# Performance work log

Measured on AMD Instinct MI355X. Metric: run time of the kernel, lower is better.

Reference implementation:

```python
import jax, jax.numpy as jnp
import numpy as np

N, E, D, L = 50000, 800000, 96, 4
IN_H, IN_E, HID, OUT = 26, 4, 128, 8
BN_EPS, AGG_EPS = 1e-5, 1e-6


def setup_inputs() -> dict:
    key = jax.random.key(0)
    ks = jax.random.split(key, 24)
    f32 = jnp.float32
    nrm = lambda k, sh, s=0.05: jax.random.normal(k, sh, f32) * s
    inp = {
        "h1": nrm(ks[0], (N, 6), 1.0),
        "h2": nrm(ks[1], (N, 4), 1.0),
        "z": nrm(ks[2], (N, 16), 1.0),
        "efeat": nrm(ks[3], (E, IN_E), 1.0),
        "max_action": jnp.ones((N, 1), f32),
        "Wh_emb": nrm(ks[4], (IN_H, D)), "bh_emb": jnp.zeros((D,), f32),
        "We_emb": nrm(ks[5], (IN_E, D)), "be_emb": jnp.zeros((D,), f32),
        "WA": nrm(ks[6], (L, D, D)), "bA": jnp.zeros((L, D), f32),
        "WB": nrm(ks[7], (L, D, D)), "bB": jnp.zeros((L, D), f32),
        "WC": nrm(ks[8], (L, D, D)), "bC": jnp.zeros((L, D), f32),
        "WD": nrm(ks[9], (L, D, D)), "bD": jnp.zeros((L, D), f32),
        "WE": nrm(ks[10], (L, D, D)), "bE": jnp.zeros((L, D), f32),
        "bn_h_g": jnp.ones((L, D), f32), "bn_h_b": jnp.zeros((L, D), f32),
        "bn_e_g": jnp.ones((L, D), f32), "bn_e_b": jnp.zeros((L, D), f32),
        "W1": nrm(ks[11], (D, HID)), "b1": jnp.zeros((HID,), f32),
        "W2": nrm(ks[12], (HID, OUT)), "b2": jnp.zeros((OUT,), f32),
        "src": jax.random.randint(ks[13], (E,), 0, N),
        "dst": jax.random.randint(ks[14], (E,), 0, N),
    }
    return inp


def _bn(x, g, b):
    # BatchNorm1d in train mode: batch stats over node/edge axis, biased var
    mu = x.mean(axis=0)
    var = x.var(axis=0)
    return g * (x - mu) * jax.lax.rsqrt(var + BN_EPS) + b


def reference(h1, h2, z, efeat, max_action, Wh_emb, bh_emb, We_emb, be_emb,
              WA, bA, WB, bB, WC, bC, WD, bD, WE, bE,
              bn_h_g, bn_h_b, bn_e_g, bn_e_b, W1, b1, W2, b2, src, dst):
    # input embedding  (Actor concat: states then z)
    h = jnp.concatenate([h1, h2, z], axis=-1) @ Wh_emb + bh_emb   # [N, D]
    e = efeat @ We_emb + be_emb                                    # [E, D]
    n = h.shape[0]
    for l in range(L):  # GatedGCN layers (residual + BN + ReLU)
        Ah = h @ WA[l] + bA[l]
        Bh = h @ WB[l] + bB[l]
        Dh = h @ WD[l] + bD[l]
        Eh = h @ WE[l] + bE[l]
        Ce = e @ WC[l] + bC[l]
        e_new = Dh[src] + Eh[dst] + Ce                             # [E, D]
        sig = jax.nn.sigmoid(e_new)
        num = jax.ops.segment_sum(sig * Bh[src], dst, num_segments=n)
        den = jax.ops.segment_sum(sig, dst, num_segments=n)
        h_new = Ah + num / (den + AGG_EPS)
        h = h + jax.nn.relu(_bn(h_new, bn_h_g[l], bn_h_b[l]))
        e = e + jax.nn.relu(_bn(e_new, bn_e_g[l], bn_e_b[l]))
    # MLP head + tanh scale
    out = jax.nn.relu(h @ W1 + b1) @ W2 + b2                        # [N, OUT]
    return max_action * jnp.tanh(out)
```

## Files before the change

kernel.cpp:

```cpp
#include <hip/hip_runtime.h>
#include <math.h>

#define NN 50000
#define EE 800000
#define DD 96
#define NHID 128
#define NOUT 8
#define LDA 104

typedef unsigned int uint32;
typedef float floatx2 __attribute__((ext_vector_type(2)));
typedef float f32x4 __attribute__((ext_vector_type(4)));
typedef short bf16x8 __attribute__((ext_vector_type(8)));

__device__ __forceinline__ float bfu2f(ushort u) {
  union { uint32 u; float f; } v; v.u = ((uint32)u) << 16; return v.f;
}
__device__ __forceinline__ ushort f2bf(float x) {
  union { float f; uint32 u; } v; v.f = x;
  uint32 r = (v.u + 0x7fffu + ((v.u >> 16) & 1u)) >> 16;
  return (ushort)r;
}

template <int ESZ> struct EST;
template <> struct EST<2> {
  static __device__ __forceinline__ float4 ld(const void* e, size_t grp) {
    const ushort4 a = ((const ushort4*)e)[grp];
    return make_float4(bfu2f(a.x), bfu2f(a.y), bfu2f(a.z), bfu2f(a.w));
  }
  static __device__ __forceinline__ void st(void* e, size_t grp, float4 v) {
    ushort4 o; o.x = f2bf(v.x); o.y = f2bf(v.y); o.z = f2bf(v.z); o.w = f2bf(v.w);
    ((ushort4*)e)[grp] = o;
  }
  static __device__ __forceinline__ float ld1c(const void* e, size_t pos, int c) {
    return bfu2f(((const ushort*)e)[pos * DD + c]);
  }
};
template <> struct EST<1> {
  static __device__ __forceinline__ float4 ld(const void* e, size_t grp) {
    const int u = ((const int*)e)[grp];
    floatx2 lo = __builtin_amdgcn_cvt_pk_f32_fp8(u, false);
    floatx2 hi = __builtin_amdgcn_cvt_pk_f32_fp8(u, true);
    return make_float4(lo[0], lo[1], hi[0], hi[1]);
  }
  static __device__ __forceinline__ void st(void* e, size_t grp, float4 v) {
    int u = 0;
    u = __builtin_amdgcn_cvt_pk_fp8_f32(v.x, v.y, u, false);
    u = __builtin_amdgcn_cvt_pk_fp8_f32(v.z, v.w, u, true);
    ((int*)e)[grp] = u;
  }
  static __device__ __forceinline__ float ld1c(const void* e, size_t pos, int c) {
    const int dw = ((const int*)e)[pos * (DD / 4) + (c >> 2)];
    floatx2 lo = __builtin_amdgcn_cvt_pk_f32_fp8(dw, false);
    floatx2 hi = __builtin_amdgcn_cvt_pk_f32_fp8(dw, true);
    return (c & 2) ? ((c & 1) ? hi[1] : hi[0]) : ((c & 1) ? lo[1] : lo[0]);
  }
};

__global__ __launch_bounds__(256) void k_zero_init(int* __restrict__ cnt,
    float* __restrict__ stats) {
  int i = blockIdx.x * 256 + threadIdx.x;
  const int str = gridDim.x * 256;
  for (; i < NN; i += str) cnt[i] = 0;
  if (blockIdx.x == 0)
    for (int j = threadIdx.x; j < 768; j += 256) stats[j] = 0.f;
}

__global__ __launch_bounds__(256) void k_hist(const int* __restrict__ dst,
    int* __restrict__ cnt) {
  const int i = blockIdx.x * 256 + threadIdx.x;
  if (i < EE) atomicAdd(&cnt[dst[i]], 1);
}

__global__ __launch_bounds__(256) void k_scan(const int* __restrict__ cnt,
    int* __restrict__ rowptr, int* __restrict__ cursor) {
  __shared__ int part[256];
  const int t = threadIdx.x;
  const int CH = (NN + 255) / 256;
  const int lo = t * CH, hi = min((t + 1) * CH, NN);
  int s = 0;
  for (int i = lo; i < hi; i++) s += cnt[i];
  part[t] = s;
  __syncthreads();
  for (int off = 1; off < 256; off <<= 1) {
    int v = (t >= off) ? part[t - off] : 0;
    __syncthreads();
    part[t] += v;
    __syncthreads();
  }
  int base = (t == 0) ? 0 : part[t - 1];
  for (int i = lo; i < hi; i++) {
    rowptr[i] = base; cursor[i] = base; base += cnt[i];
  }
  if (t == 255) rowptr[NN] = base;
}

__global__ __launch_bounds__(256) void k_scatter(const int* __restrict__ src,
    const int* __restrict__ dst, int* __restrict__ cursor,
    int* __restrict__ perm, int* __restrict__ srcC, int* __restrict__ dstC) {
  const int i = blockIdx.x * 256 + threadIdx.x;
  if (i < EE) {
    const int d = dst[i];
    const int pos = atomicAdd(&cursor[d], 1);
    perm[pos] = i; srcC[pos] = src[i]; dstC[pos] = d;
  }
}

__global__ __launch_bounds__(256) void k_embed_h(const float* __restrict__ h1,
    const float* __restrict__ h2, const float* __restrict__ z,
    const float* __restrict__ W, const float* __restrict__ b,
    ushort* __restrict__ h) {
  int idx = blockIdx.x * 256 + threadIdx.x;
  const int total = NN * DD;
  const int stride = gridDim.x * 256;
  for (; idx < total; idx += stride) {
    int n = idx / DD, c = idx - n * DD;
    float acc = b[c];
#pragma unroll
    for (int k = 0; k < 6; k++)  acc = fmaf(h1[n * 6 + k], W[k * DD + c], acc);
#pragma unroll
    for (int k = 0; k < 4; k++)  acc = fmaf(h2[n * 4 + k], W[(6 + k) * DD + c], acc);
#pragma unroll
    for (int k = 0; k < 16; k++) acc = fmaf(z[n * 16 + k], W[(10 + k) * DD + c], acc);
    h[idx] = f2bf(acc);
  }
}

template <int EZ>
__global__ __launch_bounds__(256) void k_embed_e(const float* __restrict__ ef,
    const float* __restrict__ W, const float* __restrict__ b,
    const int* __restrict__ perm, void* __restrict__ e) {
  int g = blockIdx.x * 256 + threadIdx.x;
  const int totalg = EE * (DD / 4);
  const int stride = gridDim.x * 256;
  for (; g < totalg; g += stride) {
    const int pos = g / 24, cg = (g - pos * 24) * 4;
    const int orig = perm[pos];
    const float f0 = ef[orig * 4], f1 = ef[orig * 4 + 1];
    const float f2 = ef[orig * 4 + 2], f3 = ef[orig * 4 + 3];
    float4 acc;
    acc.x = b[cg+0] + f0*W[cg+0] + f1*W[DD+cg+0] + f2*W[2*DD+cg+0] + f3*W[3*DD+cg+0];
    acc.y = b[cg+1] + f0*W[cg+1] + f1*W[DD+cg+1] + f2*W[2*DD+cg+1] + f3*W[3*DD+cg+1];
    acc.z = b[cg+2] + f0*W[cg+2] + f1*W[DD+cg+2] + f2*W[2*DD+cg+2] + f3*W[3*DD+cg+2];
    acc.w = b[cg+3] + f0*W[cg+3] + f1*W[DD+cg+3] + f2*W[2*DD+cg+3] + f3*W[3*DD+cg+3];
    EST<EZ>::st(e, g, acc);
  }
}

__global__ __launch_bounds__(256) void k_ngemm(const ushort* __restrict__ h,
    const float* __restrict__ WAp, const float* __restrict__ WBp,
    const float* __restrict__ WDp, const float* __restrict__ WEp,
    const float* __restrict__ bAp, const float* __restrict__ bBp,
    const float* __restrict__ bDp, const float* __restrict__ bEp,
    ushort* __restrict__ oA, ushort* __restrict__ oB,
    ushort* __restrict__ oD, ushort* __restrict__ oE) {
  const float* W; const float* bias; ushort* out;
  const int m = blockIdx.y;
  if (m == 0)      { W = WAp; bias = bAp; out = oA; }
  else if (m == 1) { W = WBp; bias = bBp; out = oB; }
  else if (m == 2) { W = WDp; bias = bDp; out = oD; }
  else             { W = WEp; bias = bEp; out = oE; }
  __shared__ __align__(16) ushort Wt[DD * LDA];
  __shared__ __align__(16) ushort At[64 * LDA];
  const int tid = threadIdx.x;
  for (int i = tid; i < DD * DD; i += 256) {
    const int k = i / DD, n = i - (i / DD) * DD;
    Wt[n * LDA + k] = f2bf(W[i]);
  }
  const int base = blockIdx.x * 64;
  for (int i = tid; i < 64 * 24; i += 256) {
    const int r = i / 24, q = i - (i / 24) * 24;
    const int row = base + r;
    ushort4 a;
    if (row < NN) a = ((const ushort4*)h)[(size_t)row * 24 + q];
    else { a.x = 0; a.y = 0; a.z = 0; a.w = 0; }
    *(ushort4*)&At[r * LDA + q * 4] = a;
  }
  __syncthreads();
  const int w = tid >> 6, lane = tid & 63;
  const int lrow = lane & 15, lgrp = lane >> 4;
  f32x4 acc[6];
#pragma unroll
  for (int nt = 0; nt < 6; nt++) { acc[nt][0]=0.f; acc[nt][1]=0.f; acc[nt][2]=0.f; acc[nt][3]=0.f; }
#pragma unroll
  for (int kk = 0; kk < 3; kk++) {
    const bf16x8 af = *(const bf16x8*)&At[(w * 16 + lrow) * LDA + kk * 32 + lgrp * 8];
#pragma unroll
    for (int nt = 0; nt < 6; nt++) {
      const bf16x8 bfr = *(const bf16x8*)&Wt[(nt * 16 + lrow) * LDA + kk * 32 + lgrp * 8];
      acc[nt] = __builtin_amdgcn_mfma_f32_16x16x32_bf16(af, bfr, acc[nt], 0, 0, 0);
    }
  }
#pragma unroll
  for (int j = 0; j < 4; j++) {
    const int row = base + w * 16 + lgrp * 4 + j;
    if (row < NN) {
#pragma unroll
      for (int nt = 0; nt < 6; nt++) {
        const int ch = nt * 16 + lrow;
        out[(size_t)row * DD + ch] = f2bf(acc[nt][j] + bias[ch]);
      }
    }
  }
}

template <int MODE, int EZE, int EZN>
__global__ __launch_bounds__(256) void k_edge(void* __restrict__ e,
    void* __restrict__ e_new,
    const float* __restrict__ WC, const float* __restrict__ bC,
    const ushort* __restrict__ Dh, const ushort* __restrict__ Eh,
    const int* __restrict__ srcC, const int* __restrict__ dstC,
    float* __restrict__ stats) {
  __shared__ __align__(16) ushort Wt[DD * LDA];
  __shared__ __align__(16) ushort At[64 * LDA];
  __shared__ float sred[2 * DD];
  __shared__ float escl[DD], eshl[DD];
  __shared__ int sidx_s[64], sidx_d[64];
  const int tid = threadIdx.x;
  for (int i = tid; i < DD * DD; i += 256) {
    const int k = i / DD, n = i - (i / DD) * DD;
    Wt[n * LDA + k] = f2bf(WC[i]);
  }
  if (tid < 2 * DD) sred[tid] = 0.f;
  if (MODE >= 1 && tid < DD) { escl[tid] = stats[576 + tid]; eshl[tid] = stats[672 + tid]; }
  __syncthreads();
  const int w = tid >> 6, lane = tid & 63;
  const int lrow = lane & 15, lgrp = lane >> 4;
  const int qq0 = lane % 24;
  const int qq1 = (lane + 16) % 24;
  const int qq2 = (lane + 8) % 24;
  const float4 bc0 = *(const float4*)&bC[qq0 * 4];
  const float4 bc1 = *(const float4*)&bC[qq1 * 4];
  const float4 bc2 = *(const float4*)&bC[qq2 * 4];
  float sacc0[4] = {0,0,0,0}, sacc1[4] = {0,0,0,0}, sacc2[4] = {0,0,0,0};
  float qacc0[4] = {0,0,0,0}, qacc1[4] = {0,0,0,0}, qacc2[4] = {0,0,0,0};

  const int NT = EE / 64;
  for (int t = blockIdx.x; t < NT; t += gridDim.x) {
    const size_t base = (size_t)t * 64;
#pragma unroll
    for (int ii = 0; ii < 6; ii++) {
      const int i = ii * 256 + tid;
      const int r = i / 24, gq = i - (i / 24) * 24;
      const size_t gi = (base + r) * 24 + gq;
      float4 a = EST<EZE>::ld(e, gi);
      if (MODE >= 1) {
        const float4 d = EST<EZN>::ld(e_new, gi);
        const int c = gq * 4;
        a.x += fmaxf(fmaf(d.x, escl[c],     eshl[c]),     0.f);
        a.y += fmaxf(fmaf(d.y, escl[c + 1], eshl[c + 1]), 0.f);
        a.z += fmaxf(fmaf(d.z, escl[c + 2], eshl[c + 2]), 0.f);
        a.w += fmaxf(fmaf(d.w, escl[c + 3], eshl[c + 3]), 0.f);
        if (MODE == 1) EST<EZE>::st(e, gi, a);
      }
      ushort4 o; o.x = f2bf(a.x); o.y = f2bf(a.y); o.z = f2bf(a.z); o.w = f2bf(a.w);
      *(ushort4*)&At[r * LDA + gq * 4] = o;
    }
    if (tid < 64) { sidx_s[tid] = srcC[base + tid]; sidx_d[tid] = dstC[base + tid]; }
    __syncthreads();
    f32x4 acc[6];
#pragma unroll
    for (int nt = 0; nt < 6; nt++) { acc[nt][0]=0.f; acc[nt][1]=0.f; acc[nt][2]=0.f; acc[nt][3]=0.f; }
#pragma unroll
    for (int kk = 0; kk < 3; kk++) {
      const bf16x8 af = *(const bf16x8*)&At[(w * 16 + lrow) * LDA + kk * 32 + lgrp * 8];
#pragma unroll
      for (int nt = 0; nt < 6; nt++) {
        const bf16x8 bfr = *(const bf16x8*)&Wt[(nt * 16 + lrow) * LDA + kk * 32 + lgrp * 8];
        acc[nt] = __builtin_amdgcn_mfma_f32_16x16x32_bf16(af, bfr, acc[nt], 0, 0, 0);
      }
    }
#pragma unroll
    for (int j = 0; j < 4; j++) {
#pragma unroll
      for (int nt = 0; nt < 6; nt++) {
        At[(w * 16 + lgrp * 4 + j) * LDA + nt * 16 + lrow] = f2bf(acc[nt][j]);
      }
    }
#pragma unroll
    for (int it = 0; it < 6; it++) {
      const int idx = it * 64 + lane;
      const int r16 = idx / 24, gq = idx - r16 * 24;
      const int row = w * 16 + r16;
      const size_t pos = base + row;
      const int s = sidx_s[row], d2 = sidx_d[row];
      const ushort4 av = *(const ushort4*)&At[row * LDA + gq * 4];
      const ushort4 dv = *(const ushort4*)&Dh[(size_t)s * DD + gq * 4];
      const ushort4 ev = *(const ushort4*)&Eh[(size_t)d2 * DD + gq * 4];
      const float4 bc = (it % 3 == 0) ? bc0 : (it % 3 == 1) ? bc1 : bc2;
      float4 v;
      v.x = bfu2f(av.x) + bc.x + bfu2f(dv.x) + bfu2f(ev.x);
      v.y = bfu2f(av.y) + bc.y + bfu2f(dv.y) + bfu2f(ev.y);
      v.z = bfu2f(av.z) + bc.z + bfu2f(dv.z) + bfu2f(ev.z);
      v.w = bfu2f(av.w) + bc.w + bfu2f(dv.w) + bfu2f(ev.w);
      if (it % 3 == 0) {
        sacc0[0]+=v.x; sacc0[1]+=v.y; sacc0[2]+=v.z; sacc0[3]+=v.w;
        qacc0[0]+=v.x*v.x; qacc0[1]+=v.y*v.y; qacc0[2]+=v.z*v.z; qacc0[3]+=v.w*v.w;
      } else if (it % 3 == 1) {
        sacc1[0]+=v.x; sacc1[1]+=v.y; sacc1[2]+=v.z; sacc1[3]+=v.w;
        qacc1[0]+=v.x*v.x; qacc1[1]+=v.y*v.y; qacc1[2]+=v.z*v.z; qacc1[3]+=v.w*v.w;
      } else {
        sacc2[0]+=v.x; sacc2[1]+=v.y; sacc2[2]+=v.z; sacc2[3]+=v.w;
        qacc2[0]+=v.x*v.x; qacc2[1]+=v.y*v.y; qacc2[2]+=v.z*v.z; qacc2[3]+=v.w*v.w;
      }
      EST<EZN>::st(e_new, pos * 24 + gq, v);
    }
    __syncthreads();
  }
#pragma unroll
  for (int c = 0; c < 4; c++) {
    atomicAdd(&sred[qq0 * 4 + c], sacc0[c]);
    atomicAdd(&sred[DD + qq0 * 4 + c], qacc0[c]);
    atomicAdd(&sred[qq1 * 4 + c], sacc1[c]);
    atomicAdd(&sred[DD + qq1 * 4 + c], qacc1[c]);
    atomicAdd(&sred[qq2 * 4 + c], sacc2[c]);
    atomicAdd(&sred[DD + qq2 * 4 + c], qacc2[c]);
  }
  __syncthreads();
  if (tid < 2 * DD) atomicAdd(&stats[tid], sred[tid]);
}

template <int EZN>
__global__ __launch_bounds__(256) void k_agg(const void* __restrict__ e_new,
    const int* __restrict__ srcC, const int* __restrict__ rowptr,
    const ushort* __restrict__ Bh, ushort* __restrict__ hn,
    float* __restrict__ stats) {
  __shared__ float sred[2 * DD];
  if (threadIdx.x < 2 * DD) sred[threadIdx.x] = 0.f;
  __syncthreads();
  const int hw = threadIdx.x >> 5, lane = threadIdx.x & 31;
  const int c0 = lane, c1 = lane + 32, c2 = lane + 64;
  float sa0 = 0, sa1 = 0, sa2 = 0, qa0 = 0, qa1 = 0, qa2 = 0;
  for (int n = blockIdx.x * 8 + hw; n < NN; n += gridDim.x * 8) {
    const int rs = rowptr[n], re = rowptr[n + 1];
    float n0 = 0, n1 = 0, n2 = 0, d0 = 0, d1 = 0, d2 = 0;
    for (int p = rs; p < re; p++) {
      const int s = srcC[p];
      const float v0 = EST<EZN>::ld1c(e_new, (size_t)p, c0);
      const float v1 = EST<EZN>::ld1c(e_new, (size_t)p, c1);
      const float v2 = EST<EZN>::ld1c(e_new, (size_t)p, c2);
      const float g0 = 1.f / (1.f + __expf(-v0));
      const float g1 = 1.f / (1.f + __expf(-v1));
      const float g2 = 1.f / (1.f + __expf(-v2));
      const size_t sb = (size_t)s * DD;
      n0 += g0 * bfu2f(Bh[sb + c0]); d0 += g0;
      n1 += g1 * bfu2f(Bh[sb + c1]); d1 += g1;
      n2 += g2 * bfu2f(Bh[sb + c2]); d2 += g2;
    }
    const size_t hb = (size_t)n * DD;
    const float v0 = bfu2f(hn[hb + c0]) + n0 / (d0 + 1e-6f);
    const float v1 = bfu2f(hn[hb + c1]) + n1 / (d1 + 1e-6f);
    const float v2 = bfu2f(hn[hb + c2]) + n2 / (d2 + 1e-6f);
    hn[hb + c0] = f2bf(v0); hn[hb + c1] = f2bf(v1); hn[hb + c2] = f2bf(v2);
    sa0 += v0; qa0 += v0 * v0;
    sa1 += v1; qa1 += v1 * v1;
    sa2 += v2; qa2 += v2 * v2;
  }
  atomicAdd(&sred[c0], sa0); atomicAdd(&sred[c1], sa1); atomicAdd(&sred[c2], sa2);
  atomicAdd(&sred[DD + c0], qa0); atomicAdd(&sred[DD + c1], qa1); atomicAdd(&sred[DD + c2], qa2);
  __syncthreads();
  if (threadIdx.x < 2 * DD) atomicAdd(&stats[192 + threadIdx.x], sred[threadIdx.x]);
}

__global__ void k_finalize(float* __restrict__ stats,
    const float* __restrict__ g_h, const float* __restrict__ b_h,
    const float* __restrict__ g_e, const float* __restrict__ b_e) {
  const int c = threadIdx.x;
  if (c < DD) {
    const float mu_h = stats[192 + c] / (float)NN;
    const float var_h = stats[288 + c] / (float)NN - mu_h * mu_h;
    const float sc_h = g_h[c] * rsqrtf(var_h + 1e-5f);
    const float mu_e = stats[c] / (float)EE;
    const float var_e = stats[96 + c] / (float)EE - mu_e * mu_e;
    const float sc_e = g_e[c] * rsqrtf(var_e + 1e-5f);
    stats[384 + c] = sc_h;
    stats[480 + c] = b_h[c] - mu_h * sc_h;
    stats[576 + c] = sc_e;
    stats[672 + c] = b_e[c] - mu_e * sc_e;
    stats[c] = 0.f; stats[96 + c] = 0.f; stats[192 + c] = 0.f; stats[288 + c] = 0.f;
  }
}

__global__ __launch_bounds__(256) void k_update_h(ushort* __restrict__ h,
    const ushort* __restrict__ hn, const float* __restrict__ stats) {
  int idx = blockIdx.x * 256 + threadIdx.x;
  const int stride = gridDim.x * 256;
  for (; idx < NN * DD; idx += stride) {
    const int c = idx % DD;
    const float v = fmaf(bfu2f(hn[idx]), stats[384 + c], stats[480 + c]);
    h[idx] = f2bf(bfu2f(h[idx]) + fmaxf(v, 0.f));
  }
}

__global__ __launch_bounds__(256) void k_head(const ushort* __restrict__ h,
    const float* __restrict__ W1, const float* __restrict__ b1,
    const float* __restrict__ W2, const float* __restrict__ b2,
    const float* __restrict__ ma, float* __restrict__ out) {
  __shared__ float W1l[DD * NHID];
  __shared__ float W2l[NHID * NOUT];
  __shared__ float hid[4][NHID];
  __shared__ float hrow[4][DD];
  for (int i = threadIdx.x; i < DD * NHID; i += 256) W1l[i] = W1[i];
  for (int i = threadIdx.x; i < NHID * NOUT; i += 256) W2l[i] = W2[i];
  __syncthreads();
  const int w = threadIdx.x >> 6, lane = threadIdx.x & 63;
  for (int n = blockIdx.x * 4 + w; n < NN; n += gridDim.x * 4) {
    const ushort* hp = h + (size_t)n * DD;
    if (lane < DD - 64) hrow[w][64 + lane] = bfu2f(hp[64 + lane]);
    hrow[w][lane] = bfu2f(hp[lane]);
    float a0 = b1[lane], a1 = b1[64 + lane];
    for (int k = 0; k < DD; k++) {
      const float x = hrow[w][k];
      a0 = fmaf(x, W1l[k * NHID + lane], a0);
      a1 = fmaf(x, W1l[k * NHID + 64 + lane], a1);
    }
    hid[w][lane] = fmaxf(a0, 0.f);
    hid[w][64 + lane] = fmaxf(a1, 0.f);
    if (lane < NOUT) {
      float o = b2[lane];
      for (int k = 0; k < NHID; k++) o = fmaf(hid[w][k], W2l[k * NOUT + lane], o);
      out[(size_t)n * NOUT + lane] = ma[n] * tanhf(o);
    }
  }
}

extern "C" void kernel_launch(void* const* d_in, const int* in_sizes, int n_in,
                              void* d_out, int out_size, void* d_ws, size_t ws_size,
                              hipStream_t stream) {
  const float* h1  = (const float*)d_in[0];
  const float* h2  = (const float*)d_in[1];
  const float* z   = (const float*)d_in[2];
  const float* ef  = (const float*)d_in[3];
  const float* ma  = (const float*)d_in[4];
  const float* Wh  = (const float*)d_in[5];
  const float* bh  = (const float*)d_in[6];
  const float* We  = (const float*)d_in[7];
  const float* be  = (const float*)d_in[8];
  const float* WA  = (const float*)d_in[9];
  const float* bA  = (const float*)d_in[10];
  const float* WB  = (const float*)d_in[11];
  const float* bB  = (const float*)d_in[12];
  const float* WC  = (const float*)d_in[13];
  const float* bC  = (const float*)d_in[14];
  const float* WD  = (const float*)d_in[15];
  const float* bD  = (const float*)d_in[16];
  const float* WE  = (const float*)d_in[17];
  const float* bE  = (const float*)d_in[18];
  const float* bn_h_g = (const float*)d_in[19];
  const float* bn_h_b = (const float*)d_in[20];
  const float* bn_e_g = (const float*)d_in[21];
  const float* bn_e_b = (const float*)d_in[22];
  const float* W1  = (const float*)d_in[23];
  const float* b1  = (const float*)d_in[24];
  const float* W2  = (const float*)d_in[25];
  const float* b2  = (const float*)d_in[26];
  const int*   src = (const int*)d_in[27];
  const int*   dst = (const int*)d_in[28];

  const size_t E_ELEMS = (size_t)EE * DD;
  const size_t N_ELEMS = (size_t)NN * DD;
  int tier;
  if (ws_size >= 455000000UL)      tier = 0;
  else if (ws_size >= 297000000UL) tier = 1;
  else                             tier = 2;
  const size_t esze = (tier == 0) ? 2 : 1;
  const size_t eszn = (tier <= 1) ? 2 : 1;

  char* p = (char*)d_ws;
  void* e     = (void*)p; p += E_ELEMS * esze;
  void* e_new = (void*)p; p += E_ELEMS * eszn;
  ushort* h   = (ushort*)p; p += N_ELEMS * 2;
  ushort* hn  = (ushort*)p; p += N_ELEMS * 2;
  ushort* Bhb = (ushort*)p; p += N_ELEMS * 2;
  ushort* Dhb = (ushort*)p; p += N_ELEMS * 2;
  ushort* Ehb = (ushort*)p; p += N_ELEMS * 2;
  int* cnt    = (int*)p; p += (size_t)NN * 4;
  int* rowptr = (int*)p; p += (size_t)(NN + 1) * 4;
  int* cursor = (int*)p; p += (size_t)NN * 4;
  int* perm   = (int*)p; p += (size_t)EE * 4;
  int* srcC   = (int*)p; p += (size_t)EE * 4;
  int* dstC   = (int*)p; p += (size_t)EE * 4;
  float* stats = (float*)p;

  k_zero_init<<<64, 256, 0, stream>>>(cnt, stats);
  k_hist<<<3125, 256, 0, stream>>>(dst, cnt);
  k_scan<<<1, 256, 0, stream>>>(cnt, rowptr, cursor);
  k_scatter<<<3125, 256, 0, stream>>>(src, dst, cursor, perm, srcC, dstC);
  k_embed_h<<<1024, 256, 0, stream>>>(h1, h2, z, Wh, bh, h);
  if (esze == 2) k_embed_e<2><<<2048, 256, 0, stream>>>(ef, We, be, perm, e);
  else           k_embed_e<1><<<2048, 256, 0, stream>>>(ef, We, be, perm, e);

  for (int l = 0; l < 4; l++) {
    dim3 gn(782, 4);
    k_ngemm<<<gn, 256, 0, stream>>>(h,
        WA + l * DD * DD, WB + l * DD * DD, WD + l * DD * DD, WE + l * DD * DD,
        bA + l * DD, bB + l * DD, bD + l * DD, bE + l * DD,
        hn, Bhb, Dhb, Ehb);
    const float* WCl = WC + l * DD * DD;
    const float* bCl = bC + l * DD;
#define EDGE_ARGS e, e_new, WCl, bCl, Dhb, Ehb, srcC, dstC, stats
    if (tier == 0) {
      if (l == 0)      k_edge<0,2,2><<<1250, 256, 0, stream>>>(EDGE_ARGS);
      else if (l < 3)  k_edge<1,2,2><<<1250, 256, 0, stream>>>(EDGE_ARGS);
      else             k_edge<2,2,2><<<1250, 256, 0, stream>>>(EDGE_ARGS);
    } else if (tier == 1) {
      if (l == 0)      k_edge<0,1,2><<<1250, 256, 0, stream>>>(EDGE_ARGS);
      else if (l < 3)  k_edge<1,1,2><<<1250, 256, 0, stream>>>(EDGE_ARGS);
      else             k_edge<2,1,2><<<1250, 256, 0, stream>>>(EDGE_ARGS);
    } else {
      if (l == 0)      k_edge<0,1,1><<<1250, 256, 0, stream>>>(EDGE_ARGS);
      else if (l < 3)  k_edge<1,1,1><<<1250, 256, 0, stream>>>(EDGE_ARGS);
      else             k_edge<2,1,1><<<1250, 256, 0, stream>>>(EDGE_ARGS);
    }
#undef EDGE_ARGS
    if (eszn == 2) k_agg<2><<<1024, 256, 0, stream>>>(e_new, srcC, rowptr, Bhb, hn, stats);
    else           k_agg<1><<<1024, 256, 0, stream>>>(e_new, srcC, rowptr, Bhb, hn, stats);
    k_finalize<<<1, 128, 0, stream>>>(stats,
        bn_h_g + l * DD, bn_h_b + l * DD, bn_e_g + l * DD, bn_e_b + l * DD);
    k_update_h<<<1024, 256, 0, stream>>>(h, hn, stats);
  }

  k_head<<<1024, 256, 0, stream>>>(h, W1, b1, W2, b2, ma, (float*)d_out);
}
```

Baseline: 2.057 ms.

## Make edge kernel wave-independent, widen edge loads, unroll aggregation loop by two

```diff
diff --git a/kernel.cpp b/kernel.cpp
--- a/kernel.cpp
+++ b/kernel.cpp
@@ -12,6 +12,7 @@
 typedef float floatx2 __attribute__((ext_vector_type(2)));
 typedef float f32x4 __attribute__((ext_vector_type(4)));
 typedef short bf16x8 __attribute__((ext_vector_type(8)));
+typedef ushort ushort8_t __attribute__((ext_vector_type(8)));
 
 __device__ __forceinline__ float bfu2f(ushort u) {
   union { uint32 u; float f; } v; v.u = ((uint32)u) << 16; return v.f;
@@ -31,6 +32,17 @@
   static __device__ __forceinline__ void st(void* e, size_t grp, float4 v) {
     ushort4 o; o.x = f2bf(v.x); o.y = f2bf(v.y); o.z = f2bf(v.z); o.w = f2bf(v.w);
     ((ushort4*)e)[grp] = o;
+  }
+  static __device__ __forceinline__ void ld8(const void* e, size_t i8, float* a) {
+    const ushort8_t u = ((const ushort8_t*)e)[i8];
+#pragma unroll
+    for (int j = 0; j < 8; j++) a[j] = bfu2f(u[j]);
+  }
+  static __device__ __forceinline__ void st8(void* e, size_t i8, const float* a) {
+    ushort8_t u;
+#pragma unroll
+    for (int j = 0; j < 8; j++) u[j] = f2bf(a[j]);
+    ((ushort8_t*)e)[i8] = u;
   }
   static __device__ __forceinline__ float ld1c(const void* e, size_t pos, int c) {
     return bfu2f(((const ushort*)e)[pos * DD + c]);
@@ -48,6 +60,26 @@
     u = __builtin_amdgcn_cvt_pk_fp8_f32(v.x, v.y, u, false);
     u = __builtin_amdgcn_cvt_pk_fp8_f32(v.z, v.w, u, true);
     ((int*)e)[grp] = u;
+  }
+  static __device__ __forceinline__ void ld8(const void* e, size_t i8, float* a) {
+    const int2 u = ((const int2*)e)[i8];
+    floatx2 l0 = __builtin_amdgcn_cvt_pk_f32_fp8(u.x, false);
+    floatx2 h0 = __builtin_amdgcn_cvt_pk_f32_fp8(u.x, true);
+    floatx2 l1 = __builtin_amdgcn_cvt_pk_f32_fp8(u.y, false);
+    floatx2 h1 = __builtin_amdgcn_cvt_pk_f32_fp8(u.y, true);
+    a[0]=l0[0]; a[1]=l0[1]; a[2]=h0[0]; a[3]=h0[1];
+    a[4]=l1[0]; a[5]=l1[1]; a[6]=h1[0]; a[7]=h1[1];
+  }
+  static __device__ __forceinline__ void st8(void* e, size_t i8, const float* a) {
+    int2 u;
+    int w0 = 0;
+    w0 = __builtin_amdgcn_cvt_pk_fp8_f32(a[0], a[1], w0, false);
+    w0 = __builtin_amdgcn_cvt_pk_fp8_f32(a[2], a[3], w0, true);
+    int w1 = 0;
+    w1 = __builtin_amdgcn_cvt_pk_fp8_f32(a[4], a[5], w1, false);
+    w1 = __builtin_amdgcn_cvt_pk_fp8_f32(a[6], a[7], w1, true);
+    u.x = w0; u.y = w1;
+    ((int2*)e)[i8] = u;
   }
   static __device__ __forceinline__ float ld1c(const void* e, size_t pos, int c) {
     const int dw = ((const int*)e)[pos * (DD / 4) + (c >> 2)];
@@ -212,10 +244,9 @@
     const int* __restrict__ srcC, const int* __restrict__ dstC,
     float* __restrict__ stats) {
   __shared__ __align__(16) ushort Wt[DD * LDA];
-  __shared__ __align__(16) ushort At[64 * LDA];
+  __shared__ __align__(16) ushort At[4][16 * LDA];
   __shared__ float sred[2 * DD];
   __shared__ float escl[DD], eshl[DD];
-  __shared__ int sidx_s[64], sidx_d[64];
   const int tid = threadIdx.x;
   for (int i = tid; i < DD * DD; i += 256) {
     const int k = i / DD, n = i - (i / DD) * DD;
@@ -235,35 +266,38 @@
   float sacc0[4] = {0,0,0,0}, sacc1[4] = {0,0,0,0}, sacc2[4] = {0,0,0,0};
   float qacc0[4] = {0,0,0,0}, qacc1[4] = {0,0,0,0}, qacc2[4] = {0,0,0,0};
 
-  const int NT = EE / 64;
-  for (int t = blockIdx.x; t < NT; t += gridDim.x) {
-    const size_t base = (size_t)t * 64;
-#pragma unroll
-    for (int ii = 0; ii < 6; ii++) {
-      const int i = ii * 256 + tid;
-      const int r = i / 24, gq = i - (i / 24) * 24;
-      const size_t gi = (base + r) * 24 + gq;
-      float4 a = EST<EZE>::ld(e, gi);
+  const int NTW = EE / 16;
+  const int gwave = blockIdx.x * 4 + w;
+  const int nwave = gridDim.x * 4;
+  for (int t = gwave; t < NTW; t += nwave) {
+    const size_t base = (size_t)t * 16;
+#pragma unroll
+    for (int it = 0; it < 3; it++) {
+      const int idx = it * 64 + lane;
+      const int r = idx / 12, g8 = idx - (idx / 12) * 12;
+      const size_t gi8 = (base + r) * 12 + g8;
+      float a[8];
+      EST<EZE>::ld8(e, gi8, a);
       if (MODE >= 1) {
-        const float4 d = EST<EZN>::ld(e_new, gi);
-        const int c = gq * 4;
-        a.x += fmaxf(fmaf(d.x, escl[c],     eshl[c]),     0.f);
-        a.y += fmaxf(fmaf(d.y, escl[c + 1], eshl[c + 1]), 0.f);
-        a.z += fmaxf(fmaf(d.z, escl[c + 2], eshl[c + 2]), 0.f);
-        a.w += fmaxf(fmaf(d.w, escl[c + 3], eshl[c + 3]), 0.f);
-        if (MODE == 1) EST<EZE>::st(e, gi, a);
+        float d[8];
+        EST<EZN>::ld8(e_new, gi8, d);
+        const int c = g8 * 8;
+#pragma unroll
+        for (int j = 0; j < 8; j++)
+          a[j] += fmaxf(fmaf(d[j], escl[c + j], eshl[c + j]), 0.f);
+        if (MODE == 1) EST<EZE>::st8(e, gi8, a);
       }
-      ushort4 o; o.x = f2bf(a.x); o.y = f2bf(a.y); o.z = f2bf(a.z); o.w = f2bf(a.w);
-      *(ushort4*)&At[r * LDA + gq * 4] = o;
-    }
-    if (tid < 64) { sidx_s[tid] = srcC[base + tid]; sidx_d[tid] = dstC[base + tid]; }
-    __syncthreads();
+      ushort8_t o;
+#pragma unroll
+      for (int j = 0; j < 8; j++) o[j] = f2bf(a[j]);
+      *(ushort8_t*)&At[w][r * LDA + g8 * 8] = o;
+    }
     f32x4 acc[6];
 #pragma unroll
     for (int nt = 0; nt < 6; nt++) { acc[nt][0]=0.f; acc[nt][1]=0.f; acc[nt][2]=0.f; acc[nt][3]=0.f; }
 #pragma unroll
     for (int kk = 0; kk < 3; kk++) {
-      const bf16x8 af = *(const bf16x8*)&At[(w * 16 + lrow) * LDA + kk * 32 + lgrp * 8];
+      const bf16x8 af = *(const bf16x8*)&At[w][lrow * LDA + kk * 32 + lgrp * 8];
 #pragma unroll
       for (int nt = 0; nt < 6; nt++) {
         const bf16x8 bfr = *(const bf16x8*)&Wt[(nt * 16 + lrow) * LDA + kk * 32 + lgrp * 8];
@@ -274,17 +308,16 @@
     for (int j = 0; j < 4; j++) {
 #pragma unroll
       for (int nt = 0; nt < 6; nt++) {
-        At[(w * 16 + lgrp * 4 + j) * LDA + nt * 16 + lrow] = f2bf(acc[nt][j]);
+        At[w][(lgrp * 4 + j) * LDA + nt * 16 + lrow] = f2bf(acc[nt][j]);
       }
     }
 #pragma unroll
     for (int it = 0; it < 6; it++) {
       const int idx = it * 64 + lane;
-      const int r16 = idx / 24, gq = idx - r16 * 24;
-      const int row = w * 16 + r16;
-      const size_t pos = base + row;
-      const int s = sidx_s[row], d2 = sidx_d[row];
-      const ushort4 av = *(const ushort4*)&At[row * LDA + gq * 4];
+      const int r16 = idx / 24, gq = idx - (idx / 24) * 24;
+      const size_t pos = base + r16;
+      const int s = srcC[pos], d2 = dstC[pos];
+      const ushort4 av = *(const ushort4*)&At[w][r16 * LDA + gq * 4];
       const ushort4 dv = *(const ushort4*)&Dh[(size_t)s * DD + gq * 4];
       const ushort4 ev = *(const ushort4*)&Eh[(size_t)d2 * DD + gq * 4];
       const float4 bc = (it % 3 == 0) ? bc0 : (it % 3 == 1) ? bc1 : bc2;
@@ -305,7 +338,6 @@
       }
       EST<EZN>::st(e_new, pos * 24 + gq, v);
     }
-    __syncthreads();
   }
 #pragma unroll
   for (int c = 0; c < 4; c++) {
@@ -334,7 +366,29 @@
   for (int n = blockIdx.x * 8 + hw; n < NN; n += gridDim.x * 8) {
     const int rs = rowptr[n], re = rowptr[n + 1];
     float n0 = 0, n1 = 0, n2 = 0, d0 = 0, d1 = 0, d2 = 0;
-    for (int p = rs; p < re; p++) {
+    int p = rs;
+    for (; p + 2 <= re; p += 2) {
+      const int sA = srcC[p], sB = srcC[p + 1];
+      const float vA0 = EST<EZN>::ld1c(e_new, (size_t)p, c0);
+      const float vA1 = EST<EZN>::ld1c(e_new, (size_t)p, c1);
+      const float vA2 = EST<EZN>::ld1c(e_new, (size_t)p, c2);
+      const float vB0 = EST<EZN>::ld1c(e_new, (size_t)(p + 1), c0);
+      const float vB1 = EST<EZN>::ld1c(e_new, (size_t)(p + 1), c1);
+      const float vB2 = EST<EZN>::ld1c(e_new, (size_t)(p + 1), c2);
+      const size_t sbA = (size_t)sA * DD, sbB = (size_t)sB * DD;
+      const float bA0 = bfu2f(Bh[sbA + c0]), bA1 = bfu2f(Bh[sbA + c1]), bA2 = bfu2f(Bh[sbA + c2]);
+      const float bB0 = bfu2f(Bh[sbB + c0]), bB1 = bfu2f(Bh[sbB + c1]), bB2 = bfu2f(Bh[sbB + c2]);
+      const float gA0 = 1.f / (1.f + __expf(-vA0));
+      const float gA1 = 1.f / (1.f + __expf(-vA1));
+      const float gA2 = 1.f / (1.f + __expf(-vA2));
+      const float gB0 = 1.f / (1.f + __expf(-vB0));
+      const float gB1 = 1.f / (1.f + __expf(-vB1));
+      const float gB2 = 1.f / (1.f + __expf(-vB2));
+      n0 += gA0 * bA0 + gB0 * bB0; d0 += gA0 + gB0;
+      n1 += gA1 * bA1 + gB1 * bB1; d1 += gA1 + gB1;
+      n2 += gA2 * bA2 + gB2 * bB2; d2 += gA2 + gB2;
+    }
+    if (p < re) {
       const int s = srcC[p];
       const float v0 = EST<EZN>::ld1c(e_new, (size_t)p, c0);
       const float v1 = EST<EZN>::ld1c(e_new, (size_t)p, c1);
@@ -500,17 +554,17 @@
     const float* bCl = bC + l * DD;
 #define EDGE_ARGS e, e_new, WCl, bCl, Dhb, Ehb, srcC, dstC, stats
     if (tier == 0) {
-      if (l == 0)      k_edge<0,2,2><<<1250, 256, 0, stream>>>(EDGE_ARGS);
-      else if (l < 3)  k_edge<1,2,2><<<1250, 256, 0, stream>>>(EDGE_ARGS);
-      else             k_edge<2,2,2><<<1250, 256, 0, stream>>>(EDGE_ARGS);
+      if (l == 0)      k_edge<0,2,2><<<2500, 256, 0, stream>>>(EDGE_ARGS);
+      else if (l < 3)  k_edge<1,2,2><<<2500, 256, 0, stream>>>(EDGE_ARGS);
+      else             k_edge<2,2,2><<<2500, 256, 0, stream>>>(EDGE_ARGS);
     } else if (tier == 1) {
-      if (l == 0)      k_edge<0,1,2><<<1250, 256, 0, stream>>>(EDGE_ARGS);
-      else if (l < 3)  k_edge<1,1,2><<<1250, 256, 0, stream>>>(EDGE_ARGS);
-      else             k_edge<2,1,2><<<1250, 256, 0, stream>>>(EDGE_ARGS);
+      if (l == 0)      k_edge<0,1,2><<<2500, 256, 0, stream>>>(EDGE_ARGS);
+      else if (l < 3)  k_edge<1,1,2><<<2500, 256, 0, stream>>>(EDGE_ARGS);
+      else             k_edge<2,1,2><<<2500, 256, 0, stream>>>(EDGE_ARGS);
     } else {
-      if (l == 0)      k_edge<0,1,1><<<1250, 256, 0, stream>>>(EDGE_ARGS);
-      else if (l < 3)  k_edge<1,1,1><<<1250, 256, 0, stream>>>(EDGE_ARGS);
-      else             k_edge<2,1,1><<<1250, 256, 0, stream>>>(EDGE_ARGS);
+      if (l == 0)      k_edge<0,1,1><<<2500, 256, 0, stream>>>(EDGE_ARGS);
+      else if (l < 3)  k_edge<1,1,1><<<2500, 256, 0, stream>>>(EDGE_ARGS);
+      else             k_edge<2,1,1><<<2500, 256, 0, stream>>>(EDGE_ARGS);
     }
 #undef EDGE_ARGS
     if (eszn == 2) k_agg<2><<<1024, 256, 0, stream>>>(e_new, srcC, rowptr, Bhb, hn, stats);
```

Result: slower. 2.949 ms (+43.4%).

## Fuse BN residual update into node GEMM and head, merge four GEMMs per block

Applied to the files above, without the earlier changes.

```diff
diff --git a/kernel.cpp b/kernel.cpp
--- a/kernel.cpp
+++ b/kernel.cpp
@@ -147,60 +147,97 @@
   }
 }
 
-__global__ __launch_bounds__(256) void k_ngemm(const ushort* __restrict__ h,
+template <int LAZY>
+__global__ __launch_bounds__(256) void k_ngemm(ushort* __restrict__ h,
     const float* __restrict__ WAp, const float* __restrict__ WBp,
     const float* __restrict__ WDp, const float* __restrict__ WEp,
     const float* __restrict__ bAp, const float* __restrict__ bBp,
     const float* __restrict__ bDp, const float* __restrict__ bEp,
     ushort* __restrict__ oA, ushort* __restrict__ oB,
-    ushort* __restrict__ oD, ushort* __restrict__ oE) {
-  const float* W; const float* bias; ushort* out;
-  const int m = blockIdx.y;
-  if (m == 0)      { W = WAp; bias = bAp; out = oA; }
-  else if (m == 1) { W = WBp; bias = bBp; out = oB; }
-  else if (m == 2) { W = WDp; bias = bDp; out = oD; }
-  else             { W = WEp; bias = bEp; out = oE; }
+    ushort* __restrict__ oD, ushort* __restrict__ oE,
+    const float* __restrict__ stats) {
   __shared__ __align__(16) ushort Wt[DD * LDA];
-  __shared__ __align__(16) ushort At[64 * LDA];
+  __shared__ __align__(16) ushort At[128 * LDA];
+  __shared__ float uscl[DD], ushf[DD];
   const int tid = threadIdx.x;
-  for (int i = tid; i < DD * DD; i += 256) {
-    const int k = i / DD, n = i - (i / DD) * DD;
-    Wt[n * LDA + k] = f2bf(W[i]);
-  }
-  const int base = blockIdx.x * 64;
-  for (int i = tid; i < 64 * 24; i += 256) {
+  if (LAZY && tid < DD) { uscl[tid] = stats[384 + tid]; ushf[tid] = stats[480 + tid]; }
+  if (LAZY) __syncthreads();
+  const int base = blockIdx.x * 128;
+#pragma unroll
+  for (int ii = 0; ii < 12; ii++) {
+    const int i = ii * 256 + tid;
     const int r = i / 24, q = i - (i / 24) * 24;
     const int row = base + r;
-    ushort4 a;
-    if (row < NN) a = ((const ushort4*)h)[(size_t)row * 24 + q];
-    else { a.x = 0; a.y = 0; a.z = 0; a.w = 0; }
+    ushort4 a; a.x = 0; a.y = 0; a.z = 0; a.w = 0;
+    if (row < NN) {
+      a = ((const ushort4*)h)[(size_t)row * 24 + q];
+      if (LAZY) {
+        const ushort4 u = ((const ushort4*)0)[0], *dummy = &u; (void)dummy;
+      }
+    }
+    if (LAZY && row < NN) {
+      const ushort4 u = ((const ushort4*)oA)[(size_t)row * 24 + q];
+      const int c = q * 4;
+      float f0 = bfu2f(a.x) + fmaxf(fmaf(bfu2f(u.x), uscl[c],     ushf[c]),     0.f);
+      float f1 = bfu2f(a.y) + fmaxf(fmaf(bfu2f(u.y), uscl[c + 1], ushf[c + 1]), 0.f);
+      float f2 = bfu2f(a.z) + fmaxf(fmaf(bfu2f(u.z), uscl[c + 2], ushf[c + 2]), 0.f);
+      float f3 = bfu2f(a.w) + fmaxf(fmaf(bfu2f(u.w), uscl[c + 3], ushf[c + 3]), 0.f);
+      a.x = f2bf(f0); a.y = f2bf(f1); a.z = f2bf(f2); a.w = f2bf(f3);
+      ((ushort4*)h)[(size_t)row * 24 + q] = a;
+    }
     *(ushort4*)&At[r * LDA + q * 4] = a;
   }
-  __syncthreads();
   const int w = tid >> 6, lane = tid & 63;
   const int lrow = lane & 15, lgrp = lane >> 4;
-  f32x4 acc[6];
-#pragma unroll
-  for (int nt = 0; nt < 6; nt++) { acc[nt][0]=0.f; acc[nt][1]=0.f; acc[nt][2]=0.f; acc[nt][3]=0.f; }
-#pragma unroll
-  for (int kk = 0; kk < 3; kk++) {
-    const bf16x8 af = *(const bf16x8*)&At[(w * 16 + lrow) * LDA + kk * 32 + lgrp * 8];
-#pragma unroll
-    for (int nt = 0; nt < 6; nt++) {
-      const bf16x8 bfr = *(const bf16x8*)&Wt[(nt * 16 + lrow) * LDA + kk * 32 + lgrp * 8];
-      acc[nt] = __builtin_amdgcn_mfma_f32_16x16x32_bf16(af, bfr, acc[nt], 0, 0, 0);
-    }
-  }
-#pragma unroll
-  for (int j = 0; j < 4; j++) {
-    const int row = base + w * 16 + lgrp * 4 + j;
-    if (row < NN) {
+#pragma unroll
+  for (int m = 0; m < 4; m++) {
+    const float* W  = (m == 0) ? WAp : (m == 1) ? WBp : (m == 2) ? WDp : WEp;
+    const float* bi = (m == 0) ? bAp : (m == 1) ? bBp : (m == 2) ? bDp : bEp;
+    ushort* out     = (m == 0) ? oA  : (m == 1) ? oB  : (m == 2) ? oD  : oE;
+#pragma unroll
+    for (int ii = 0; ii < 36; ii++) {
+      const int i = ii * 256 + tid;
+      const int k = i / DD, n = i - (i / DD) * DD;
+      Wt[n * LDA + k] = f2bf(W[i]);
+    }
+    __syncthreads();
+    f32x4 acc[2][6];
+#pragma unroll
+    for (int rt2 = 0; rt2 < 2; rt2++)
 #pragma unroll
       for (int nt = 0; nt < 6; nt++) {
-        const int ch = nt * 16 + lrow;
-        out[(size_t)row * DD + ch] = f2bf(acc[nt][j] + bias[ch]);
-      }
-    }
+        acc[rt2][nt][0] = 0.f; acc[rt2][nt][1] = 0.f;
+        acc[rt2][nt][2] = 0.f; acc[rt2][nt][3] = 0.f;
+      }
+#pragma unroll
+    for (int rt2 = 0; rt2 < 2; rt2++) {
+      const int rt = w * 2 + rt2;
+#pragma unroll
+      for (int kk = 0; kk < 3; kk++) {
+        const bf16x8 af = *(const bf16x8*)&At[(rt * 16 + lrow) * LDA + kk * 32 + lgrp * 8];
+#pragma unroll
+        for (int nt = 0; nt < 6; nt++) {
+          const bf16x8 bfr = *(const bf16x8*)&Wt[(nt * 16 + lrow) * LDA + kk * 32 + lgrp * 8];
+          acc[rt2][nt] = __builtin_amdgcn_mfma_f32_16x16x32_bf16(af, bfr, acc[rt2][nt], 0, 0, 0);
+        }
+      }
+    }
+#pragma unroll
+    for (int rt2 = 0; rt2 < 2; rt2++) {
+      const int rt = w * 2 + rt2;
+#pragma unroll
+      for (int j = 0; j < 4; j++) {
+        const int row = base + rt * 16 + lgrp * 4 + j;
+        if (row < NN) {
+#pragma unroll
+          for (int nt = 0; nt < 6; nt++) {
+            const int ch = nt * 16 + lrow;
+            out[(size_t)row * DD + ch] = f2bf(acc[rt2][nt][j] + bi[ch]);
+          }
+        }
+      }
+    }
+    __syncthreads();
   }
 }
 
@@ -280,7 +317,7 @@
 #pragma unroll
     for (int it = 0; it < 6; it++) {
       const int idx = it * 64 + lane;
-      const int r16 = idx / 24, gq = idx - r16 * 24;
+      const int r16 = idx / 24, gq = idx - (idx / 24) * 24;
       const int row = w * 16 + r16;
       const size_t pos = base + row;
       const int s = sidx_s[row], d2 = sidx_d[row];
@@ -334,7 +371,29 @@
   for (int n = blockIdx.x * 8 + hw; n < NN; n += gridDim.x * 8) {
     const int rs = rowptr[n], re = rowptr[n + 1];
     float n0 = 0, n1 = 0, n2 = 0, d0 = 0, d1 = 0, d2 = 0;
-    for (int p = rs; p < re; p++) {
+    int p = rs;
+    for (; p + 2 <= re; p += 2) {
+      const int sA = srcC[p], sB = srcC[p + 1];
+      const float vA0 = EST<EZN>::ld1c(e_new, (size_t)p, c0);
+      const float vA1 = EST<EZN>::ld1c(e_new, (size_t)p, c1);
+      const float vA2 = EST<EZN>::ld1c(e_new, (size_t)p, c2);
+      const float vB0 = EST<EZN>::ld1c(e_new, (size_t)(p + 1), c0);
+      const float vB1 = EST<EZN>::ld1c(e_new, (size_t)(p + 1), c1);
+      const float vB2 = EST<EZN>::ld1c(e_new, (size_t)(p + 1), c2);
+      const size_t sbA = (size_t)sA * DD, sbB = (size_t)sB * DD;
+      const float bA0 = bfu2f(Bh[sbA + c0]), bA1 = bfu2f(Bh[sbA + c1]), bA2 = bfu2f(Bh[sbA + c2]);
+      const float bB0 = bfu2f(Bh[sbB + c0]), bB1 = bfu2f(Bh[sbB + c1]), bB2 = bfu2f(Bh[sbB + c2]);
+      const float gA0 = 1.f / (1.f + __expf(-vA0));
+      const float gA1 = 1.f / (1.f + __expf(-vA1));
+      const float gA2 = 1.f / (1.f + __expf(-vA2));
+      const float gB0 = 1.f / (1.f + __expf(-vB0));
+      const float gB1 = 1.f / (1.f + __expf(-vB1));
+      const float gB2 = 1.f / (1.f + __expf(-vB2));
+      n0 += gA0 * bA0 + gB0 * bB0; d0 += gA0 + gB0;
+      n1 += gA1 * bA1 + gB1 * bB1; d1 += gA1 + gB1;
+      n2 += gA2 * bA2 + gB2 * bB2; d2 += gA2 + gB2;
+    }
+    if (p < re) {
       const int s = srcC[p];
       const float v0 = EST<EZN>::ld1c(e_new, (size_t)p, c0);
       const float v1 = EST<EZN>::ld1c(e_new, (size_t)p, c1);
@@ -381,18 +440,8 @@
   }
 }
 
-__global__ __launch_bounds__(256) void k_update_h(ushort* __restrict__ h,
-    const ushort* __restrict__ hn, const float* __restrict__ stats) {
-  int idx = blockIdx.x * 256 + threadIdx.x;
-  const int stride = gridDim.x * 256;
-  for (; idx < NN * DD; idx += stride) {
-    const int c = idx % DD;
-    const float v = fmaf(bfu2f(hn[idx]), stats[384 + c], stats[480 + c]);
-    h[idx] = f2bf(bfu2f(h[idx]) + fmaxf(v, 0.f));
-  }
-}
-
 __global__ __launch_bounds__(256) void k_head(const ushort* __restrict__ h,
+    const ushort* __restrict__ hn, const float* __restrict__ stats,
     const float* __restrict__ W1, const float* __restrict__ b1,
     const float* __restrict__ W2, const float* __restrict__ b2,
     const float* __restrict__ ma, float* __restrict__ out) {
@@ -400,14 +449,23 @@
   __shared__ float W2l[NHID * NOUT];
   __shared__ float hid[4][NHID];
   __shared__ float hrow[4][DD];
+  __shared__ float uscl[DD], ushf[DD];
   for (int i = threadIdx.x; i < DD * NHID; i += 256) W1l[i] = W1[i];
   for (int i = threadIdx.x; i < NHID * NOUT; i += 256) W2l[i] = W2[i];
+  if (threadIdx.x < DD) {
+    uscl[threadIdx.x] = stats[384 + threadIdx.x];
+    ushf[threadIdx.x] = stats[480 + threadIdx.x];
+  }
   __syncthreads();
   const int w = threadIdx.x >> 6, lane = threadIdx.x & 63;
   for (int n = blockIdx.x * 4 + w; n < NN; n += gridDim.x * 4) {
     const ushort* hp = h + (size_t)n * DD;
-    if (lane < DD - 64) hrow[w][64 + lane] = bfu2f(hp[64 + lane]);
-    hrow[w][lane] = bfu2f(hp[lane]);
+    const ushort* up = hn + (size_t)n * DD;
+    hrow[w][lane] = bfu2f(hp[lane])
+        + fmaxf(fmaf(bfu2f(up[lane]), uscl[lane], ushf[lane]), 0.f);
+    if (lane < DD - 64)
+      hrow[w][64 + lane] = bfu2f(hp[64 + lane])
+          + fmaxf(fmaf(bfu2f(up[64 + lane]), uscl[64 + lane], ushf[64 + lane]), 0.f);
     float a0 = b1[lane], a1 = b1[64 + lane];
     for (int k = 0; k < DD; k++) {
       const float x = hrow[w][k];
@@ -491,11 +549,11 @@
   else           k_embed_e<1><<<2048, 256, 0, stream>>>(ef, We, be, perm, e);
 
   for (int l = 0; l < 4; l++) {
-    dim3 gn(782, 4);
-    k_ngemm<<<gn, 256, 0, stream>>>(h,
-        WA + l * DD * DD, WB + l * DD * DD, WD + l * DD * DD, WE + l * DD * DD,
-        bA + l * DD, bB + l * DD, bD + l * DD, bE + l * DD,
-        hn, Bhb, Dhb, Ehb);
+#define NG_ARGS h, WA + l*DD*DD, WB + l*DD*DD, WD + l*DD*DD, WE + l*DD*DD, \
+    bA + l*DD, bB + l*DD, bD + l*DD, bE + l*DD, hn, Bhb, Dhb, Ehb, stats
+    if (l == 0) k_ngemm<0><<<391, 256, 0, stream>>>(NG_ARGS);
+    else        k_ngemm<1><<<391, 256, 0, stream>>>(NG_ARGS);
+#undef NG_ARGS
     const float* WCl = WC + l * DD * DD;
     const float* bCl = bC + l * DD;
 #define EDGE_ARGS e, e_new, WCl, bCl, Dhb, Ehb, srcC, dstC, stats
@@ -517,8 +575,7 @@
     else           k_agg<1><<<1024, 256, 0, stream>>>(e_new, srcC, rowptr, Bhb, hn, stats);
     k_finalize<<<1, 128, 0, stream>>>(stats,
         bn_h_g + l * DD, bn_h_b + l * DD, bn_e_g + l * DD, bn_e_b + l * DD);
-    k_update_h<<<1024, 256, 0, stream>>>(h, hn, stats);
-  }
-
-  k_head<<<1024, 256, 0, stream>>>(h, W1, b1, W2, b2, ma, (float*)d_out);
-}
+  }
+
+  k_head<<<1024, 256, 0, stream>>>(h, hn, stats, W1, b1, W2, b2, ma, (float*)d_out);
+}
```

Result: faster. 1.963 ms (-4.6%).
